# Performance work log

Hardware: AMD Instinct MI355X
Metric: run time of the kernel (lower is better)

Reference implementation:

```python
import jax, jax.numpy as jnp
import numpy as np

DEPTH, DIM, HEADS, EXP = 6, 768, 12, 4
B, N = 8, 1024
EPS = 1e-5


def setup_inputs() -> dict:
    key = jax.random.key(0)
    ks = jax.random.split(key, 6)
    s = 0.02
    inp = {
        "x": jax.random.normal(ks[0], (B, N, DIM), dtype=jnp.float32),
        "ln1_g": jnp.ones((DEPTH, DIM), jnp.float32),
        "ln1_b": jnp.zeros((DEPTH, DIM), jnp.float32),
        "wqkv": jax.random.normal(ks[1], (DEPTH, DIM, 3 * DIM), jnp.float32) * s,
        "bqkv": jnp.zeros((DEPTH, 3 * DIM), jnp.float32),
        "ln2_g": jnp.ones((DEPTH, DIM), jnp.float32),
        "ln2_b": jnp.zeros((DEPTH, DIM), jnp.float32),
        "w1": jax.random.normal(ks[2], (DEPTH, DIM, EXP * DIM), jnp.float32) * s,
        "b1": jnp.zeros((DEPTH, EXP * DIM), jnp.float32),
        "w2": jax.random.normal(ks[3], (DEPTH, EXP * DIM, DIM), jnp.float32) * s,
        "b2": jnp.zeros((DEPTH, DIM), jnp.float32),
    }
    return inp


def _layernorm(x, g, b):
    mu = jnp.mean(x, axis=-1, keepdims=True)
    var = jnp.mean(jnp.square(x - mu), axis=-1, keepdims=True)
    return (x - mu) * jax.lax.rsqrt(var + EPS) * g + b


def _block(x, p):
    ln1_g, ln1_b, wqkv, bqkv, ln2_g, ln2_b, w1, b1, w2, b2 = p
    # --- attention (pre-norm, residual) ---
    x1 = _layernorm(x, ln1_g, ln1_b)
    qkv = x1 @ wqkv + bqkv  # [b, n, 3*dim]
    q, k, v = jnp.split(qkv, 3, axis=-1)
    dh = DIM // HEADS
    def heads(t):  # b n (h d) -> b h n d
        return t.reshape(B, N, HEADS, dh).transpose(0, 2, 1, 3)
    q, k, v = heads(q), heads(k), heads(v)
    scale = DIM ** (-0.5)  # NB: module scales by full dim, not head dim
    dots = jnp.einsum("bhnd,bhmd->bhnm", q, k) * scale
    attn = jax.nn.softmax(dots, axis=-1)
    out = jnp.einsum("bhnm,bhmd->bhnd", attn, v)
    out = out.transpose(0, 2, 1, 3).reshape(B, N, DIM)
    x = x + out
    # --- feedforward (pre-norm, residual) ---
    x2 = _layernorm(x, ln2_g, ln2_b)
    h = jax.nn.gelu(x2 @ w1 + b1, approximate=False)
    x = x + (h @ w2 + b2)
    return x


def reference(x, ln1_g, ln1_b, wqkv, bqkv, ln2_g, ln2_b, w1, b1, w2, b2):
    params = (ln1_g, ln1_b, wqkv, bqkv, ln2_g, ln2_b, w1, b1, w2, b2)

    def body(carry, p):
        return _block(carry, p), None

    x, _ = jax.lax.scan(body, x, params)
    return x
```

## Files before the change

kernel.cpp:

```cpp
#include <hip/hip_runtime.h>
#include <hip/hip_bf16.h>
#include <math.h>

#define DEPTH 6
#define DIM   768
#define HEADS 12
#define DH    64
#define NCTX  1024
#define BATCH 8
#define ROWS  (BATCH*NCTX)
#define DIM3  (3*DIM)
#define DIMF  (4*DIM)
#define LNEPS 1e-5f

typedef __attribute__((ext_vector_type(8)))  short short8;
typedef __attribute__((ext_vector_type(4)))  float floatx4;
typedef __attribute__((ext_vector_type(16))) float floatx16;
using bf16 = __hip_bfloat16;
typedef unsigned int u32;

static __device__ __forceinline__ bf16 f2bf(float v){ return __float2bfloat16(v); }
static __device__ __forceinline__ float bf2f(unsigned short u){
    union { unsigned int i; float f; } c; c.i = ((unsigned int)u) << 16; return c.f;
}
static __device__ __forceinline__ unsigned short bfu(float v){ return __bfloat16_as_ushort(f2bf(v)); }
static __device__ __forceinline__ u32 pk2(float a, float b){
    return (u32)bfu(a) | ((u32)bfu(b) << 16);
}

static __device__ __forceinline__ void gl_lds16(const void* g, void* l) {
    __builtin_amdgcn_global_load_lds((const __attribute__((address_space(1))) void*)g,
                                     (__attribute__((address_space(3))) void*)l, 16, 0, 0);
}

__global__ void k_transpose_convert(const float* __restrict__ W, bf16* __restrict__ WT,
                                    int K, int N) {
    __shared__ float tile[32][33];
    int l = blockIdx.z;
    const float* Wl = W + (size_t)l * K * N;
    bf16* WTl = WT + (size_t)l * K * N;
    int n0 = blockIdx.x * 32, k0 = blockIdx.y * 32;
    int tx = threadIdx.x, ty = threadIdx.y;
#pragma unroll
    for (int i = 0; i < 4; i++)
        tile[ty + i*8][tx] = Wl[(size_t)(k0 + ty + i*8) * N + n0 + tx];
    __syncthreads();
#pragma unroll
    for (int i = 0; i < 4; i++)
        WTl[(size_t)(n0 + ty + i*8) * K + k0 + tx] = f2bf(tile[tx][ty + i*8]);
}

__global__ __launch_bounds__(256) void k_layernorm(const float* __restrict__ x,
                                                   const float* __restrict__ g,
                                                   const float* __restrict__ b,
                                                   bf16* __restrict__ y) {
    int row  = blockIdx.x * 4 + (threadIdx.x >> 6);
    int lane = threadIdx.x & 63;
    const float4* xr = (const float4*)(x + (size_t)row * DIM);
    float4 v[3];
    float s = 0.f, s2 = 0.f;
#pragma unroll
    for (int i = 0; i < 3; i++) {
        v[i] = xr[lane + i*64];
        s  += v[i].x + v[i].y + v[i].z + v[i].w;
        s2 += v[i].x*v[i].x + v[i].y*v[i].y + v[i].z*v[i].z + v[i].w*v[i].w;
    }
#pragma unroll
    for (int m = 1; m < 64; m <<= 1) { s += __shfl_xor(s, m); s2 += __shfl_xor(s2, m); }
    float mu  = s * (1.f / DIM);
    float var = s2 * (1.f / DIM) - mu * mu;
    float rs  = rsqrtf(var + LNEPS);
    bf16* yr = y + (size_t)row * DIM;
    const float4* g4 = (const float4*)g;
    const float4* b4 = (const float4*)b;
#pragma unroll
    for (int i = 0; i < 3; i++) {
        float4 gg = g4[lane + i*64], bb = b4[lane + i*64];
        float r0 = (v[i].x - mu) * rs * gg.x + bb.x;
        float r1 = (v[i].y - mu) * rs * gg.y + bb.y;
        float r2 = (v[i].z - mu) * rs * gg.z + bb.z;
        float r3 = (v[i].w - mu) * rs * gg.w + bb.w;
        uint2 u; u.x = pk2(r0, r1); u.y = pk2(r2, r3);
        *(uint2*)&yr[4 * (lane + i*64)] = u;
    }
}

template<int MODE, int BM, int BN>
__global__ __launch_bounds__(256, 2) void k_gemm(const bf16* __restrict__ A,
                                                 const bf16* __restrict__ WT,
                                                 const float* __restrict__ bias,
                                                 bf16* __restrict__ outb,
                                                 float* __restrict__ outf,
                                                 int N, int K) {
    constexpr int IF  = BM / 32;
    constexpr int JF  = BN / 32;
    constexpr int LPT = BM / 64 + BN / 64;
    __shared__ __align__(16) bf16 As[3][BM*32];
    __shared__ __align__(16) bf16 Bs[3][BN*32];
    int nt = N / BN;
    int nwg = gridDim.x;
    int fblk = blockIdx.x;
    int swz = (fblk & 7) * (nwg >> 3) + (fblk >> 3);
    int m0 = (swz / nt) * BM, n0 = (swz % nt) * BN;
    int t = threadIdx.x;
    int lane = t & 63, w = t >> 6;
    int wr = (w >> 1) * (BM / 2), wc = (w & 1) * (BN / 2);
    int lr = lane & 15, lg = lane >> 4;

    floatx4 acc[IF][JF] = {};
    int NT = K >> 5;

    auto STAGE = [&](int ks, int buf) {
        int ko = ks << 5;
#pragma unroll
        for (int ac = 0; ac < BM/64; ac++) {
            int c = ac*256 + t;
            int row = c >> 2, col = (c & 3) * 8;
            gl_lds16(A + (size_t)(m0 + row) * K + ko + col, &As[buf][c * 8]);
        }
#pragma unroll
        for (int bc = 0; bc < BN/64; bc++) {
            int c = bc*256 + t;
            int row = c >> 2, col = (c & 3) * 8;
            gl_lds16(WT + (size_t)(n0 + row) * K + ko + col, &Bs[buf][c * 8]);
        }
    };
    auto WAITC = [&]() {
        if constexpr (LPT == 6)      asm volatile("s_waitcnt vmcnt(6)" ::: "memory");
        else if constexpr (LPT == 4) asm volatile("s_waitcnt vmcnt(4)" ::: "memory");
        else                         asm volatile("s_waitcnt vmcnt(3)" ::: "memory");
    };

    STAGE(0, 0);
    STAGE(1, 1);
    WAITC();
    __builtin_amdgcn_s_barrier();

    for (int kb = 0; kb < NT; kb += 3) {
#pragma unroll
        for (int s = 0; s < 3; s++) {
            int ks = kb + s;
            bool pf = (ks + 2) < NT;
            if (pf) STAGE(ks + 2, (s + 2) % 3);
            short8 af[IF], bfr[JF];
#pragma unroll
            for (int i = 0; i < IF; i++) af[i]  = *(const short8*)&As[s][(wr + i*16 + lr)*32 + lg*8];
#pragma unroll
            for (int j = 0; j < JF; j++) bfr[j] = *(const short8*)&Bs[s][(wc + j*16 + lr)*32 + lg*8];
#pragma unroll
            for (int i = 0; i < IF; i++)
#pragma unroll
                for (int j = 0; j < JF; j++)
                    acc[i][j] = __builtin_amdgcn_mfma_f32_16x16x32_bf16(af[i], bfr[j], acc[i][j], 0, 0, 0);
            if (pf) WAITC();
            else    asm volatile("s_waitcnt vmcnt(0)" ::: "memory");
            __builtin_amdgcn_s_barrier();
        }
    }
#pragma unroll
    for (int i = 0; i < IF; i++)
#pragma unroll
        for (int j = 0; j < JF; j++)
#pragma unroll
            for (int r = 0; r < 4; r++) {
                int row = m0 + wr + i*16 + lg*4 + r;
                int col = n0 + wc + j*16 + lr;
                float vv = acc[i][j][r] + bias[col];
                if (MODE == 0) {
                    outb[(size_t)row * N + col] = f2bf(vv);
                } else if (MODE == 1) {
                    float u = 1.5957691216f * (vv + 0.044715f * vv * vv * vv);
                    float gs = 1.f / (1.f + __expf(-u));
                    outb[(size_t)row * N + col] = f2bf(vv * gs);
                } else {
                    outf[(size_t)row * N + col] += vv;
                }
            }
}

static __device__ __forceinline__ int vt_off(int d, int k) {
    int dw = d * 36 + (k >> 1);
    dw ^= (d & 0x38) >> 1;
    return dw * 2 + (k & 1);
}

__global__ __launch_bounds__(256, 3) void k_attn(const bf16* __restrict__ qkv,
                                                 float* __restrict__ x) {
    int f = blockIdx.x;
    int b  = f & 7;
    int rr = f >> 3;
    int h  = rr % 12;
    int qt = rr / 12;
    int t = threadIdx.x, lane = t & 63, w = t >> 6;
    int q = lane & 31, hi = lane >> 5;
    const size_t bn0 = (size_t)b * NCTX;
    const bf16* Qg = qkv + bn0 * DIM3 + h * DH;
    const bf16* Kg = Qg + DIM;
    const bf16* Vg = Qg + 2 * DIM;
    int q0 = qt * 128 + w * 32;

    const float qs = 0.036084391824351615f * 1.4426950408889634f;
    short8 qf[4];
#pragma unroll
    for (int s = 0; s < 4; s++) {
        short8 raw = *(const short8*)&Qg[(size_t)(q0 + q) * DIM3 + s*16 + hi*8];
        short8 o;
#pragma unroll
        for (int e = 0; e < 8; e++)
            o[e] = (short)bfu(bf2f((unsigned short)raw[e]) * qs);
        qf[s] = o;
    }

    __shared__ __align__(16) bf16 KsS[64*64];
    __shared__ __align__(16) bf16 VTs[64*72];
    __shared__ __align__(16) bf16 PsS[4][32*64];
    __shared__ float wbc[4][32];

    u32* ksw = (u32*)KsS;
    u32* psw = (u32*)&PsS[w][0];

    int sr[2], sc[2];
#pragma unroll
    for (int it = 0; it < 2; it++) { int c = it*256 + t; sr[it] = c >> 3; sc[it] = (c & 7) * 8; }

    floatx16 pacc[2] = {};
    float mrow = -3e38f, lrow = 0.f;

    uint4 kreg[2], vreg[2];
#pragma unroll
    for (int it = 0; it < 2; it++) {
        kreg[it] = *(const uint4*)&Kg[(size_t)sr[it] * DIM3 + sc[it]];
        vreg[it] = *(const uint4*)&Vg[(size_t)sr[it] * DIM3 + sc[it]];
    }

    for (int kt = 0; kt < 16; kt++) {
        __syncthreads();
#pragma unroll
        for (int it = 0; it < 2; it++) {
            int row = sr[it], u = sc[it] >> 3;
            *(uint4*)(ksw + row*32 + ((u ^ (row & 7)) << 2)) = kreg[it];
            const bf16* vp = (const bf16*)&vreg[it];
#pragma unroll
            for (int e = 0; e < 8; e++) VTs[vt_off(sc[it] + e, row)] = vp[e];
        }
        __syncthreads();
        if (kt + 1 < 16) {
            int kv0 = (kt + 1) * 64;
#pragma unroll
            for (int it = 0; it < 2; it++) {
                kreg[it] = *(const uint4*)&Kg[(size_t)(kv0 + sr[it]) * DIM3 + sc[it]];
                vreg[it] = *(const uint4*)&Vg[(size_t)(kv0 + sr[it]) * DIM3 + sc[it]];
            }
        }

        floatx16 sacc[2] = {};
#pragma unroll
        for (int kb = 0; kb < 2; kb++) {
#pragma unroll
            for (int s = 0; s < 4; s++) {
                int row = kb*32 + q;
                short8 kf = *(const short8*)(ksw + row*32 + (((2*s + hi) ^ (row & 7)) << 2));
                sacc[kb] = __builtin_amdgcn_mfma_f32_32x32x16_bf16(kf, qf[s], sacc[kb], 0, 0, 0);
            }
        }

        float mx = sacc[0][0];
#pragma unroll
        for (int r = 1; r < 16; r++) mx = fmaxf(mx, sacc[0][r]);
#pragma unroll
        for (int r = 0; r < 16; r++) mx = fmaxf(mx, sacc[1][r]);
        mx = fmaxf(mx, __shfl_xor(mx, 32));
        bool chg = mx > mrow + 8.f;
        if (__any(chg)) {
            float mnew = chg ? mx : mrow;
            float corr = exp2f(mrow - mnew);
            mrow = mnew;
            lrow *= corr;
            wbc[w][q] = corr;
#pragma unroll
            for (int r = 0; r < 16; r++) {
                float c = wbc[w][(r & 3) + 8*(r >> 2) + 4*hi];
                pacc[0][r] *= c; pacc[1][r] *= c;
            }
        }
        float sum = 0.f;
#pragma unroll
        for (int kb = 0; kb < 2; kb++) {
#pragma unroll
            for (int m = 0; m < 4; m++) {
                float p0 = exp2f(sacc[kb][4*m+0] - mrow);
                float p1 = exp2f(sacc[kb][4*m+1] - mrow);
                float p2 = exp2f(sacc[kb][4*m+2] - mrow);
                float p3 = exp2f(sacc[kb][4*m+3] - mrow);
                sum += (p0 + p1) + (p2 + p3);
                uint2 d2; d2.x = pk2(p0, p1); d2.y = pk2(p2, p3);
                *(uint2*)(psw + q*32 + (((m + 4*kb) ^ (q & 7)) << 2) + 2*hi) = d2;
            }
        }
        sum += __shfl_xor(sum, 32);
        lrow += sum;

#pragma unroll
        for (int ks = 0; ks < 4; ks++) {
            short8 pa = *(const short8*)(psw + q*32 + (((2*ks + hi) ^ (q & 7)) << 2));
#pragma unroll
            for (int db = 0; db < 2; db++) {
                short8 vb = *(const short8*)&VTs[vt_off(db*32 + q, 16*ks + 8*hi)];
                pacc[db] = __builtin_amdgcn_mfma_f32_32x32x16_bf16(pa, vb, pacc[db], 0, 0, 0);
            }
        }
    }

    wbc[w][q] = 1.f / lrow;
    float* xr = x + bn0 * DIM + (size_t)h * DH;
#pragma unroll
    for (int r = 0; r < 16; r++) {
        int qrow = (r & 3) + 8*(r >> 2) + 4*hi;
        float li = wbc[w][qrow];
#pragma unroll
        for (int db = 0; db < 2; db++) {
            int col = db*32 + q;
            xr[(size_t)(q0 + qrow) * DIM + col] += pacc[db][r] * li;
        }
    }
}

extern "C" void kernel_launch(void* const* d_in, const int* in_sizes, int n_in,
                              void* d_out, int out_size, void* d_ws, size_t ws_size,
                              hipStream_t stream) {
    const float* x_in  = (const float*)d_in[0];
    const float* ln1_g = (const float*)d_in[1];
    const float* ln1_b = (const float*)d_in[2];
    const float* wqkv  = (const float*)d_in[3];
    const float* bqkv  = (const float*)d_in[4];
    const float* ln2_g = (const float*)d_in[5];
    const float* ln2_b = (const float*)d_in[6];
    const float* w1    = (const float*)d_in[7];
    const float* b1    = (const float*)d_in[8];
    const float* w2    = (const float*)d_in[9];
    const float* b2    = (const float*)d_in[10];
    float* x = (float*)d_out;

    char* ws = (char*)d_ws;
    size_t off = 0;
    auto alloc = [&](size_t bytes) { void* p = ws + off; off += (bytes + 255) & ~255ull; return p; };
    bf16* wqkvT = (bf16*)alloc((size_t)DEPTH * DIM * DIM3 * 2);
    bf16* w1T   = (bf16*)alloc((size_t)DEPTH * DIM * DIMF * 2);
    bf16* w2T   = (bf16*)alloc((size_t)DEPTH * DIMF * DIM * 2);
    bf16* xn    = (bf16*)alloc((size_t)ROWS * DIM * 2);
    bf16* qkvh  = (bf16*)alloc((size_t)ROWS * DIMF * 2);
    if (off > ws_size) return;

    hipMemcpyAsync(x, x_in, (size_t)ROWS * DIM * 4, hipMemcpyDeviceToDevice, stream);

    k_transpose_convert<<<dim3(DIM3/32, DIM/32,  DEPTH), dim3(32, 8), 0, stream>>>(wqkv, wqkvT, DIM,  DIM3);
    k_transpose_convert<<<dim3(DIMF/32, DIM/32,  DEPTH), dim3(32, 8), 0, stream>>>(w1,   w1T,   DIM,  DIMF);
    k_transpose_convert<<<dim3(DIM/32,  DIMF/32, DEPTH), dim3(32, 8), 0, stream>>>(w2,   w2T,   DIMF, DIM);

    for (int l = 0; l < DEPTH; l++) {
        k_layernorm<<<ROWS/4, 256, 0, stream>>>(x, ln1_g + l*DIM, ln1_b + l*DIM, xn);
        k_gemm<0,256,128><<<dim3((DIM3/128)*(ROWS/256)), 256, 0, stream>>>(
            xn, wqkvT + (size_t)l*DIM*DIM3, bqkv + (size_t)l*DIM3, qkvh, nullptr, DIM3, DIM);
        k_attn<<<dim3(768), 256, 0, stream>>>(qkvh, x);
        k_layernorm<<<ROWS/4, 256, 0, stream>>>(x, ln2_g + l*DIM, ln2_b + l*DIM, xn);
        k_gemm<1,256,128><<<dim3((DIMF/128)*(ROWS/256)), 256, 0, stream>>>(
            xn, w1T + (size_t)l*DIM*DIMF, b1 + (size_t)l*DIMF, qkvh, nullptr, DIMF, DIM);
        k_gemm<2,128,64><<<dim3((DIM/64)*(ROWS/128)), 256, 0, stream>>>(
            qkvh, w2T + (size_t)l*DIMF*DIM, b2 + (size_t)l*DIM, nullptr, x, DIM, DIMF);
    }
}
```

Measured before the change: 1.649 ms.

## Keep attention probabilities in registers via permlane32 swap and add MFMA priority hints

The attention kernel no longer writes the softmax probabilities to shared memory and reads them back as MFMA operands. It packs them to bf16 and rearranges them across lanes with v_permlane32_swap so they can feed the PV MFMA directly. This drops the per-wave P scratch buffer in LDS and the LDS round trip on every key tile. Separately, s_setprio is raised around MFMA bursts in both the GEMM and attention kernels to favour issuing matrix work. The cost is a correctness risk in the lane mapping, and the permlane32 swap instruction is only available on newer CDNA parts.

```diff
diff --git a/kernel.cpp b/kernel.cpp
--- a/kernel.cpp
+++ b/kernel.cpp
@@ -147,11 +147,13 @@
             for (int i = 0; i < IF; i++) af[i]  = *(const short8*)&As[s][(wr + i*16 + lr)*32 + lg*8];
 #pragma unroll
             for (int j = 0; j < JF; j++) bfr[j] = *(const short8*)&Bs[s][(wc + j*16 + lr)*32 + lg*8];
+            __builtin_amdgcn_s_setprio(1);
 #pragma unroll
             for (int i = 0; i < IF; i++)
 #pragma unroll
                 for (int j = 0; j < JF; j++)
                     acc[i][j] = __builtin_amdgcn_mfma_f32_16x16x32_bf16(af[i], bfr[j], acc[i][j], 0, 0, 0);
+            __builtin_amdgcn_s_setprio(0);
             if (pf) WAITC();
             else    asm volatile("s_waitcnt vmcnt(0)" ::: "memory");
             __builtin_amdgcn_s_barrier();
@@ -213,11 +215,9 @@
 
     __shared__ __align__(16) bf16 KsS[64*64];
     __shared__ __align__(16) bf16 VTs[64*72];
-    __shared__ __align__(16) bf16 PsS[4][32*64];
     __shared__ float wbc[4][32];
 
     u32* ksw = (u32*)KsS;
-    u32* psw = (u32*)&PsS[w][0];
 
     int sr[2], sc[2];
 #pragma unroll
@@ -254,6 +254,7 @@
         }
 
         floatx16 sacc[2] = {};
+        __builtin_amdgcn_s_setprio(1);
 #pragma unroll
         for (int kb = 0; kb < 2; kb++) {
 #pragma unroll
@@ -263,6 +264,7 @@
                 sacc[kb] = __builtin_amdgcn_mfma_f32_32x32x16_bf16(kf, qf[s], sacc[kb], 0, 0, 0);
             }
         }
+        __builtin_amdgcn_s_setprio(0);
 
         float mx = sacc[0][0];
 #pragma unroll
@@ -283,32 +285,35 @@
                 pacc[0][r] *= c; pacc[1][r] *= c;
             }
         }
+
         float sum = 0.f;
 #pragma unroll
         for (int kb = 0; kb < 2; kb++) {
-#pragma unroll
-            for (int m = 0; m < 4; m++) {
-                float p0 = exp2f(sacc[kb][4*m+0] - mrow);
-                float p1 = exp2f(sacc[kb][4*m+1] - mrow);
-                float p2 = exp2f(sacc[kb][4*m+2] - mrow);
-                float p3 = exp2f(sacc[kb][4*m+3] - mrow);
-                sum += (p0 + p1) + (p2 + p3);
-                uint2 d2; d2.x = pk2(p0, p1); d2.y = pk2(p2, p3);
-                *(uint2*)(psw + q*32 + (((m + 4*kb) ^ (q & 7)) << 2) + 2*hi) = d2;
+            float pf[16];
+#pragma unroll
+            for (int r = 0; r < 16; r++) { pf[r] = exp2f(sacc[kb][r] - mrow); sum += pf[r]; }
+#pragma unroll
+            for (int g = 0; g < 2; g++) {
+                u32 a0 = pk2(pf[8*g+0], pf[8*g+1]);
+                u32 a1 = pk2(pf[8*g+2], pf[8*g+3]);
+                u32 b0 = pk2(pf[8*g+4], pf[8*g+5]);
+                u32 b1 = pk2(pf[8*g+6], pf[8*g+7]);
+                asm volatile("v_permlane32_swap_b32 %0, %1" : "+v"(a0), "+v"(b0));
+                asm volatile("v_permlane32_swap_b32 %0, %1" : "+v"(a1), "+v"(b1));
+                union { u32 u[4]; short8 s8; } pa;
+                pa.u[0] = a0; pa.u[1] = a1; pa.u[2] = b0; pa.u[3] = b1;
+                int ks = 2*kb + g;
+                __builtin_amdgcn_s_setprio(1);
+#pragma unroll
+                for (int db = 0; db < 2; db++) {
+                    short8 vb = *(const short8*)&VTs[vt_off(db*32 + q, 16*ks + 8*hi)];
+                    pacc[db] = __builtin_amdgcn_mfma_f32_32x32x16_bf16(pa.s8, vb, pacc[db], 0, 0, 0);
+                }
+                __builtin_amdgcn_s_setprio(0);
             }
         }
         sum += __shfl_xor(sum, 32);
         lrow += sum;
-
-#pragma unroll
-        for (int ks = 0; ks < 4; ks++) {
-            short8 pa = *(const short8*)(psw + q*32 + (((2*ks + hi) ^ (q & 7)) << 2));
-#pragma unroll
-            for (int db = 0; db < 2; db++) {
-                short8 vb = *(const short8*)&VTs[vt_off(db*32 + q, 16*ks + 8*hi)];
-                pacc[db] = __builtin_amdgcn_mfma_f32_32x32x16_bf16(pa, vb, pacc[db], 0, 0, 0);
-            }
-        }
     }
 
     wbc[w][q] = 1.f / lrow;
```

Result: no change. 1.619 ms (-1.8%).
